# Kernel tuning notes

Measured on AMD Instinct MI355X. Metric: run time of the kernel, lower is better.

The kernel has to match this reference:

```python
import jax, jax.numpy as jnp
import numpy as np
import math

D_MODEL = 1024
N_HEAD = 16          # sub-heads per branch
N_BR = 4             # hardcoded n_branches
DH = D_MODEL // N_HEAD
H_TOT = N_BR * N_HEAD
B, T = 1, 1024
SCALE = math.pi / math.sqrt(3.0)
ATTNSCALE = DH ** -0.5


def _rope(x):
    # x: [B, H, T, D]; matches torch RoPE: even/odd split, concat halves
    t_len, d = x.shape[2], x.shape[-1]
    inv_freq = 1.0 / (10000.0 ** (jnp.arange(0, d, 2, dtype=jnp.float32) / d))
    freqs = jnp.arange(t_len, dtype=jnp.float32)[:, None] * inv_freq[None, :]  # [T, D/2]
    cos, sin = jnp.cos(freqs), jnp.sin(freqs)
    x1, x2 = x[..., 0::2], x[..., 1::2]
    return jnp.concatenate([-x2 * sin + x1 * cos, x1 * sin + x2 * cos], axis=-1)


def setup_inputs() -> dict:
    key = jax.random.key(0)
    ks = jax.random.split(key, 12)
    s = D_MODEL ** -0.5
    return {
        "X": jax.random.normal(ks[0], (B, T, D_MODEL), jnp.float32),
        "W_Q": jax.random.normal(ks[1], (D_MODEL, D_MODEL * N_BR), jnp.float32) * s,
        "b_Q": jax.random.normal(ks[2], (D_MODEL * N_BR,), jnp.float32) * 0.02,
        "W_K": jax.random.normal(ks[3], (D_MODEL, D_MODEL), jnp.float32) * s,
        "b_K": jax.random.normal(ks[4], (D_MODEL,), jnp.float32) * 0.02,
        "W_V": jax.random.normal(ks[5], (D_MODEL, D_MODEL), jnp.float32) * s,
        "b_V": jax.random.normal(ks[6], (D_MODEL,), jnp.float32) * 0.02,
        "sink_scalars": jax.random.uniform(ks[7], (H_TOT,), jnp.float32, 0.0, 0.1),
        "v_nulls": jax.random.normal(ks[8], (N_BR, D_MODEL), jnp.float32) * 0.02,
        "W_O": jax.random.normal(ks[9], (N_BR, D_MODEL, D_MODEL), jnp.float32) * s,
        "W_O_bias": jax.random.normal(ks[10], (N_BR, D_MODEL), jnp.float32) * 0.02,
    }


def reference(X, W_Q, b_Q, W_K, b_K, W_V, b_V, sink_scalars, v_nulls, W_O, W_O_bias):
    Bv, Tv, C = X.shape
    # projections -> [B, H, T, Dh]
    q = (X @ W_Q + b_Q).reshape(Bv, Tv, H_TOT, DH).transpose(0, 2, 1, 3)
    k_base = (X @ W_K + b_K).reshape(Bv, Tv, N_HEAD, DH).transpose(0, 2, 1, 3)
    v_base = (X @ W_V + b_V).reshape(Bv, Tv, N_HEAD, DH).transpose(0, 2, 1, 3)
    k = jnp.tile(k_base, (1, N_BR, 1, 1))
    v = jnp.tile(v_base, (1, N_BR, 1, 1))
    q, k = _rope(q), _rope(k)

    scores = jnp.einsum("bhtd,bhsd->bhts", q, k) * ATTNSCALE
    key_self = jnp.clip(jnp.sum(k * k, axis=-1), 1e-6, None)      # [B,H,S]
    w = jax.nn.softplus(scores / jnp.sqrt(key_self)[:, :, None, :])
    causal = jnp.tril(jnp.ones((Tv, Tv), bool))                    # [T,S]
    w = jnp.where(causal, w, 0.0)
    w = w * jax.nn.sigmoid(SCALE * w)
    sinks = sink_scalars.reshape(1, H_TOT, 1, 1)
    w = jnp.where(w < sinks, 0.0, w)
    # concat-with-sink renormalization, expressed without the concat
    total = jnp.sum(w, axis=-1, keepdims=True) + sinks + 1e-6      # [B,H,T,1]
    probs_tokens = w / total
    probs_sink = sinks / total                                     # [B,H,T,1]

    out = jnp.einsum("bhts,bhsd->bhtd", probs_tokens, v)
    v_null = v_nulls.reshape(H_TOT, DH)[None, :, None, :]          # [1,H,1,Dh]
    out = out + probs_sink * v_null

    context = out.reshape(Bv, N_BR, N_HEAD, Tv, DH).transpose(0, 1, 3, 2, 4)
    context = context.reshape(Bv, N_BR, Tv, C)
    y = jnp.einsum("bntc,ncd->bntd", context, W_O) + W_O_bias[None, :, None, :]
    return y.mean(axis=1)
```

## Files before the change

kernel.cpp:

```cpp
#include <hip/hip_runtime.h>
#include <math.h>

typedef __attribute__((ext_vector_type(4))) float  f32x4;
typedef __attribute__((ext_vector_type(8))) short  bf16x8;
typedef __attribute__((ext_vector_type(4))) short  s16x4;

#define SQUISH_SCALE 1.8137993642342178f

__device__ __forceinline__ float b2f(short u) {
    union { float f; unsigned b; } v; v.b = ((unsigned)(unsigned short)u) << 16; return v.f;
}
__device__ __forceinline__ short f2b(float f) {
    union { float f; unsigned b; } v; v.f = f;
    unsigned r = (v.b + 0x7FFFu + ((v.b >> 16) & 1u)) >> 16;
    return (short)r;
}
__device__ __forceinline__ unsigned cvt_pk_bf16(float lo, float hi) {
    unsigned r;
    asm("v_cvt_pk_bf16_f32 %0, %1, %2" : "=v"(r) : "v"(lo), "v"(hi));
    return r;
}
__device__ __forceinline__ void gll16(const void* g, void* l) {
    __builtin_amdgcn_global_load_lds((const __attribute__((address_space(1))) void*)g,
                                     (__attribute__((address_space(3))) void*)l, 16, 0, 0);
}
__device__ __forceinline__ void gll4(const void* g, void* l) {
    __builtin_amdgcn_global_load_lds((const __attribute__((address_space(1))) void*)g,
                                     (__attribute__((address_space(3))) void*)l, 4, 0, 0);
}

__device__ __forceinline__ void do_transpose(const float* __restrict__ src, int R, int C,
                                             short* __restrict__ dst, float scale,
                                             int c0, int r0, float (*tile)[65], int tid) {
    #pragma unroll
    for (int it = 0; it < 4; ++it) {
        int lin = it * 256 + tid;
        int r = lin >> 4, c4 = lin & 15;
        f32x4 v = *(const f32x4*)(src + (size_t)(r0 + r) * C + c0 + c4 * 4);
        #pragma unroll
        for (int k = 0; k < 4; ++k) tile[r][c4 * 4 + k] = v[k];
    }
    __syncthreads();
    #pragma unroll
    for (int it = 0; it < 4; ++it) {
        int lin = it * 256 + tid;
        int c = lin >> 4, rq = lin & 15;
        s16x4 o;
        #pragma unroll
        for (int k = 0; k < 4; ++k) o[k] = f2b(tile[rq * 4 + k][c] * scale);
        *(s16x4*)(dst + (size_t)(c0 + c) * R + r0 + rq * 4) = o;
    }
}

__global__ __launch_bounds__(256) void prep_kernel(
    const float* __restrict__ X, const float* __restrict__ W_Q, const float* __restrict__ W_K,
    const float* __restrict__ W_V, const float* __restrict__ W_O,
    const float* __restrict__ bQ, const float* __restrict__ bK, const float* __restrict__ bV,
    const float* __restrict__ bO,
    short* __restrict__ Xb, short* __restrict__ WbT, short* __restrict__ WoT,
    float* __restrict__ biasQKV, float* __restrict__ out) {
    __shared__ float tile[64][65];
    const int bid = blockIdx.x, tid = threadIdx.x;
    if (bid < 256) {
        int i = (bid * 256 + tid) * 16;
        #pragma unroll
        for (int k = 0; k < 4; ++k) {
            f32x4 v = *(const f32x4*)(X + i + k * 4);
            s16x4 o;
            o.x = f2b(v.x); o.y = f2b(v.y); o.z = f2b(v.z); o.w = f2b(v.w);
            *(s16x4*)(Xb + i + k * 4) = o;
        }
    } else if (bid < 1280) {
        int b2 = bid - 256;
        do_transpose(W_Q, 1024, 4096, WbT, 1.f, (b2 & 63) * 64, (b2 >> 6) * 64, tile, tid);
    } else if (bid < 1536) {
        int b2 = bid - 1280;
        do_transpose(W_K, 1024, 1024, WbT + 4096 * 1024, 1.f, (b2 & 15) * 64, (b2 >> 4) * 64, tile, tid);
    } else if (bid < 1792) {
        int b2 = bid - 1536;
        do_transpose(W_V, 1024, 1024, WbT + 5120 * 1024, 1.f, (b2 & 15) * 64, (b2 >> 4) * 64, tile, tid);
    } else if (bid < 2816) {
        int b2 = bid - 1792;
        do_transpose(W_O, 4096, 1024, WoT, 0.25f, (b2 & 15) * 64, (b2 >> 4) * 64, tile, tid);
    } else if (bid < 2840) {
        int i = (bid - 2816) * 256 + tid;
        if (i < 4096)      biasQKV[i] = bQ[i];
        else if (i < 5120) biasQKV[i] = bK[i - 4096];
        else               biasQKV[i] = bV[i - 5120];
    } else {
        int i = ((bid - 2840) * 256 + tid) * 4;
        f32x4 v;
        #pragma unroll
        for (int k = 0; k < 4; ++k) {
            int c = (i + k) & 1023;
            v[k] = 0.25f * (bO[c] + bO[1024 + c] + bO[2048 + c] + bO[3072 + c]);
        }
        *(f32x4*)(out + i) = v;
    }
}

__global__ __launch_bounds__(256) void gemm_bt_kernel(
    const short* __restrict__ A, const short* __restrict__ BT,
    const float* __restrict__ bias, short* __restrict__ outB,
    int M, int N, int K) {
    __shared__ short lA[2][128][64];
    __shared__ short lB[2][128][64];
    const int tid = threadIdx.x;
    const int lane = tid & 63, wave = tid >> 6;
    const int l15 = lane & 15, l4 = lane >> 4;
    const int wr = wave >> 1, wc = wave & 1;
    const int n0 = blockIdx.x * 128, m0 = blockIdx.y * 128;

    f32x4 acc[4][4];
    const f32x4 fz = {0.f, 0.f, 0.f, 0.f};
    #pragma unroll
    for (int m = 0; m < 4; ++m)
        #pragma unroll
        for (int n = 0; n < 4; ++n) acc[m][n] = fz;

#define GSTAGE(k0_, b_) do {                                                   \
    _Pragma("unroll")                                                          \
    for (int it = 0; it < 4; ++it) {                                           \
        int lin0 = it * 256 + wave * 64;                                       \
        int lin = lin0 + lane;                                                 \
        int r = lin >> 3, c = (lin & 7) ^ (r & 7);                             \
        gll16(A  + (size_t)(m0 + r) * K + (k0_) + c * 8, (char*)lA[b_] + lin0 * 16); \
        gll16(BT + (size_t)(n0 + r) * K + (k0_) + c * 8, (char*)lB[b_] + lin0 * 16); \
    } } while (0)

    GSTAGE(0, 0);
    int cur = 0;
    for (int k0 = 0; k0 < K; k0 += 64) {
        if (k0 + 64 < K) {
            GSTAGE(k0 + 64, cur ^ 1);
            asm volatile("s_waitcnt vmcnt(8) lgkmcnt(0)" ::: "memory");
        } else {
            asm volatile("s_waitcnt vmcnt(0) lgkmcnt(0)" ::: "memory");
        }
        __builtin_amdgcn_s_barrier();
        #pragma unroll
        for (int kk = 0; kk < 2; ++kk) {
            bf16x8 af[4], bf_[4];
            #pragma unroll
            for (int m = 0; m < 4; ++m) {
                int row = wr * 64 + m * 16 + l15;
                int ch = (kk * 4 + l4) ^ (row & 7);
                af[m] = *(const bf16x8*)&lA[cur][row][ch << 3];
            }
            #pragma unroll
            for (int n = 0; n < 4; ++n) {
                int row = wc * 64 + n * 16 + l15;
                int ch = (kk * 4 + l4) ^ (row & 7);
                bf_[n] = *(const bf16x8*)&lB[cur][row][ch << 3];
            }
            #pragma unroll
            for (int m = 0; m < 4; ++m)
                #pragma unroll
                for (int n = 0; n < 4; ++n)
                    acc[m][n] = __builtin_amdgcn_mfma_f32_16x16x32_bf16(af[m], bf_[n], acc[m][n], 0, 0, 0);
        }
        asm volatile("" ::: "memory");
        __builtin_amdgcn_s_barrier();
        cur ^= 1;
    }
#undef GSTAGE
    #pragma unroll
    for (int m = 0; m < 4; ++m)
        #pragma unroll
        for (int n = 0; n < 4; ++n)
            #pragma unroll
            for (int r = 0; r < 4; ++r) {
                int row = m0 + wr * 64 + m * 16 + l4 * 4 + r;
                int col = n0 + wc * 64 + n * 16 + l15;
                outB[(size_t)row * N + col] = f2b(acc[m][n][r] + bias[col]);
            }
}

__global__ __launch_bounds__(256) void gemm_bt_splitk_kernel(
    const short* __restrict__ A, const short* __restrict__ BT,
    float* __restrict__ out, int M, int N, int K, int KSLICE) {
    __shared__ short lA[2][128][64];
    __shared__ short lB[2][128][64];
    const int tid = threadIdx.x;
    const int lane = tid & 63, wave = tid >> 6;
    const int l15 = lane & 15, l4 = lane >> 4;
    const int wr = wave >> 1, wc = wave & 1;
    const int n0 = blockIdx.x * 128, m0 = blockIdx.y * 128;
    const int kbeg = blockIdx.z * KSLICE, kend = kbeg + KSLICE;

    f32x4 acc[4][4];
    const f32x4 fz = {0.f, 0.f, 0.f, 0.f};
    #pragma unroll
    for (int m = 0; m < 4; ++m)
        #pragma unroll
        for (int n = 0; n < 4; ++n) acc[m][n] = fz;

#define GSTAGE(k0_, b_) do {                                                   \
    _Pragma("unroll")                                                          \
    for (int it = 0; it < 4; ++it) {                                           \
        int lin0 = it * 256 + wave * 64;                                       \
        int lin = lin0 + lane;                                                 \
        int r = lin >> 3, c = (lin & 7) ^ (r & 7);                             \
        gll16(A  + (size_t)(m0 + r) * K + (k0_) + c * 8, (char*)lA[b_] + lin0 * 16); \
        gll16(BT + (size_t)(n0 + r) * K + (k0_) + c * 8, (char*)lB[b_] + lin0 * 16); \
    } } while (0)

    GSTAGE(kbeg, 0);
    int cur = 0;
    for (int k0 = kbeg; k0 < kend; k0 += 64) {
        if (k0 + 64 < kend) {
            GSTAGE(k0 + 64, cur ^ 1);
            asm volatile("s_waitcnt vmcnt(8) lgkmcnt(0)" ::: "memory");
        } else {
            asm volatile("s_waitcnt vmcnt(0) lgkmcnt(0)" ::: "memory");
        }
        __builtin_amdgcn_s_barrier();
        #pragma unroll
        for (int kk = 0; kk < 2; ++kk) {
            bf16x8 af[4], bf_[4];
            #pragma unroll
            for (int m = 0; m < 4; ++m) {
                int row = wr * 64 + m * 16 + l15;
                int ch = (kk * 4 + l4) ^ (row & 7);
                af[m] = *(const bf16x8*)&lA[cur][row][ch << 3];
            }
            #pragma unroll
            for (int n = 0; n < 4; ++n) {
                int row = wc * 64 + n * 16 + l15;
                int ch = (kk * 4 + l4) ^ (row & 7);
                bf_[n] = *(const bf16x8*)&lB[cur][row][ch << 3];
            }
            #pragma unroll
            for (int m = 0; m < 4; ++m)
                #pragma unroll
                for (int n = 0; n < 4; ++n)
                    acc[m][n] = __builtin_amdgcn_mfma_f32_16x16x32_bf16(af[m], bf_[n], acc[m][n], 0, 0, 0);
        }
        asm volatile("" ::: "memory");
        __builtin_amdgcn_s_barrier();
        cur ^= 1;
    }
#undef GSTAGE
    #pragma unroll
    for (int m = 0; m < 4; ++m)
        #pragma unroll
        for (int n = 0; n < 4; ++n)
            #pragma unroll
            for (int r = 0; r < 4; ++r) {
                int row = m0 + wr * 64 + m * 16 + l4 * 4 + r;
                int col = n0 + wc * 64 + n * 16 + l15;
                unsafeAtomicAdd(&out[(size_t)row * N + col], acc[m][n][r]);
            }
}

__global__ __launch_bounds__(256) void rope_vt_kernel(short* __restrict__ QKVb,
                                                      float* __restrict__ ksr,
                                                      short* __restrict__ Vtb) {
    __shared__ short tile[64][72];
    const int bid = blockIdx.x, tid = threadIdx.x;
    if (bid < 1280) {
        int base = bid * 256 + tid;
        #pragma unroll
        for (int it = 0; it < 8; ++it) {
            int item = base + it * 327680;
            int j = item & 31;
            int rem = item >> 5;
            int head = rem % 80;
            int t = rem / 80;
            short* p;
            if (head < 64) p = QKVb + (size_t)t * 6144 + head * 64;
            else           p = QKVb + (size_t)t * 6144 + 4096 + (head - 64) * 64;
            float x1 = b2f(p[2 * j]), x2 = b2f(p[2 * j + 1]);
            float freq = (float)t * __builtin_exp2f(-(float)j * 0.41524101186092033f);
            float sn = __sinf(freq), cs = __cosf(freq);
            float o1 = x1 * cs - x2 * sn;
            float o2 = x1 * sn + x2 * cs;
            p[j]      = f2b(o1);
            p[32 + j] = f2b(o2);
            if (head >= 64) {
                float ss = o1 * o1 + o2 * o2;
                #pragma unroll
                for (int off = 16; off; off >>= 1) ss += __shfl_xor(ss, off, 32);
                if (j == 0) ksr[(head - 64) * 1024 + t] = 0.125f * rsqrtf(fmaxf(ss, 1e-6f));
            }
        }
    } else {
        int b2 = bid - 1280;
        int h = b2 >> 4, t0 = (b2 & 15) * 64;
        #pragma unroll
        for (int it = 0; it < 16; ++it) {
            int lin = it * 256 + tid;
            int r = lin >> 6, d = lin & 63;
            tile[r][d] = QKVb[(size_t)(t0 + r) * 6144 + 5120 + h * 64 + d];
        }
        __syncthreads();
        #pragma unroll
        for (int it = 0; it < 16; ++it) {
            int lin = it * 256 + tid;
            int d = lin >> 6, c = lin & 63;
            Vtb[(size_t)(h * 64 + d) * 1024 + t0 + c] = tile[c][d];
        }
    }
}

__global__ __launch_bounds__(256, 3) void attn_kernel(
    const short* __restrict__ QKVb, const short* __restrict__ Vtb,
    const float* __restrict__ ksr, const float* __restrict__ sinks,
    const float* __restrict__ vnulls, short* __restrict__ Ob) {
    __shared__ short lK[2][64][64];
    __shared__ short lV[2][64][64];
    __shared__ float lks[2][64];
    __shared__ float lvn[64];
    __shared__ short lP[4][16][64];

    const int tid = threadIdx.x;
    const int lane = tid & 63, wave = tid >> 6;
    const int l15 = lane & 15, l4 = lane >> 4;
    const int h = blockIdx.x;
    const int qt = 15 - blockIdx.y;
    const int h16 = h & 15;
    const int t0 = qt * 64;
    const float sink = sinks[h];
    if (tid < 64) lvn[tid] = vnulls[h * 64 + tid];

    const int q_abs = t0 + wave * 16 + l15;
    bf16x8 aq[2];
    #pragma unroll
    for (int kk = 0; kk < 2; ++kk)
        aq[kk] = *(const bf16x8*)(QKVb + (size_t)q_abs * 6144 + h * 64 + kk * 32 + l4 * 8);

    const f32x4 fz = {0.f, 0.f, 0.f, 0.f};
    f32x4 acc_o[4];
    #pragma unroll
    for (int n = 0; n < 4; ++n) acc_o[n] = fz;
    float tot = 0.f;

#define ASTAGE(s0_, b_) do {                                                          \
    int lin0 = wave * 64;                                                             \
    int lin = lin0 + lane;                                                            \
    int r = lin >> 3, c = (lin & 7) ^ (r & 7);                                        \
    gll16(QKVb + (size_t)((s0_) + r) * 6144 + 4096 + h16 * 64 + c * 8, (char*)lK[b_] + lin0 * 16); \
    gll16(Vtb + (size_t)(h16 * 64 + r) * 1024 + (s0_) + c * 8,         (char*)lV[b_] + lin0 * 16); \
    lin0 += 256; lin = lin0 + lane; r = lin >> 3; c = (lin & 7) ^ (r & 7);            \
    gll16(QKVb + (size_t)((s0_) + r) * 6144 + 4096 + h16 * 64 + c * 8, (char*)lK[b_] + lin0 * 16); \
    gll16(Vtb + (size_t)(h16 * 64 + r) * 1024 + (s0_) + c * 8,         (char*)lV[b_] + lin0 * 16); \
    gll4(ksr + h16 * 1024 + (s0_) + lane, (char*)lks[b_]);                            \
} while (0)

    const int nkt = qt + 1;
    ASTAGE(0, 0);
    int cur = 0;
    for (int kt = 0; kt < nkt; ++kt) {
        int s0 = kt * 64;
        if (kt + 1 < nkt) {
            ASTAGE(s0 + 64, cur ^ 1);
            asm volatile("s_waitcnt vmcnt(5) lgkmcnt(0)" ::: "memory");
        } else {
            asm volatile("s_waitcnt vmcnt(0) lgkmcnt(0)" ::: "memory");
        }
        __builtin_amdgcn_s_barrier();

        f32x4 accs[4];
        #pragma unroll
        for (int n = 0; n < 4; ++n) accs[n] = fz;
        #pragma unroll
        for (int kk = 0; kk < 2; ++kk) {
            bf16x8 bk[4];
            #pragma unroll
            for (int n = 0; n < 4; ++n) {
                int row = n * 16 + l15;
                int ch = (kk * 4 + l4) ^ (row & 7);
                bk[n] = *(const bf16x8*)&lK[cur][row][ch << 3];
            }
            #pragma unroll
            for (int n = 0; n < 4; ++n)
                accs[n] = __builtin_amdgcn_mfma_f32_16x16x32_bf16(bk[n], aq[kk], accs[n], 0, 0, 0);
        }

        #pragma unroll
        for (int n = 0; n < 4; ++n) {
            f32x4 ksv = *(const f32x4*)&lks[cur][n * 16 + l4 * 4];
            float w4[4];
            #pragma unroll
            for (int r = 0; r < 4; ++r) {
                int k_abs = s0 + n * 16 + l4 * 4 + r;
                float z = accs[n][r] * ksv[r];
                float e = __expf(-fabsf(z));
                float w = fmaxf(z, 0.f) + __logf(1.f + e);
                w = (k_abs <= q_abs) ? w : 0.f;
                float g = __expf(-SQUISH_SCALE * w);
                w = w * __builtin_amdgcn_rcpf(1.f + g);
                w = (w >= sink) ? w : 0.f;
                tot += w;
                w4[r] = w;
            }
            unsigned pa = cvt_pk_bf16(w4[0], w4[1]);
            unsigned pb = cvt_pk_bf16(w4[2], w4[3]);
            int ch = (2 * n + (l4 >> 1)) ^ (l15 & 7);
            uint2 val; val.x = pa; val.y = pb;
            *(uint2*)&lP[wave][l15][ch * 8 + (l4 & 1) * 4] = val;
        }

        #pragma unroll
        for (int kk = 0; kk < 2; ++kk) {
            bf16x8 ap = *(const bf16x8*)&lP[wave][l15][((kk * 4 + l4) ^ (l15 & 7)) << 3];
            bf16x8 bv[4];
            #pragma unroll
            for (int n = 0; n < 4; ++n) {
                int row = n * 16 + l15;
                int ch = (kk * 4 + l4) ^ (row & 7);
                bv[n] = *(const bf16x8*)&lV[cur][row][ch << 3];
            }
            #pragma unroll
            for (int n = 0; n < 4; ++n)
                acc_o[n] = __builtin_amdgcn_mfma_f32_16x16x32_bf16(ap, bv[n], acc_o[n], 0, 0, 0);
        }
        asm volatile("" ::: "memory");
        __builtin_amdgcn_s_barrier();
        cur ^= 1;
    }
#undef ASTAGE

    tot += __shfl_xor(tot, 16, 64);
    tot += __shfl_xor(tot, 32, 64);
    float tq[4];
    #pragma unroll
    for (int r = 0; r < 4; ++r) tq[r] = __shfl(tot, l4 * 4 + r, 64);

    #pragma unroll
    for (int r = 0; r < 4; ++r) {
        float inv = __builtin_amdgcn_rcpf(tq[r] + sink + 1e-6f);
        int trow = t0 + wave * 16 + l4 * 4 + r;
        #pragma unroll
        for (int n = 0; n < 4; ++n) {
            int d = n * 16 + l15;
            float val = (acc_o[n][r] + sink * lvn[d]) * inv;
            Ob[(size_t)trow * 4096 + h * 64 + d] = f2b(val);
        }
    }
}

extern "C" void kernel_launch(void* const* d_in, const int* in_sizes, int n_in,
                              void* d_out, int out_size, void* d_ws, size_t ws_size,
                              hipStream_t stream) {
    const float* X        = (const float*)d_in[0];
    const float* W_Q      = (const float*)d_in[1];
    const float* b_Q      = (const float*)d_in[2];
    const float* W_K      = (const float*)d_in[3];
    const float* b_K      = (const float*)d_in[4];
    const float* W_V      = (const float*)d_in[5];
    const float* b_V      = (const float*)d_in[6];
    const float* sinks    = (const float*)d_in[7];
    const float* v_nulls  = (const float*)d_in[8];
    const float* W_O      = (const float*)d_in[9];
    const float* W_O_bias = (const float*)d_in[10];
    float* out = (float*)d_out;
    char* ws = (char*)d_ws;

    short* Xb        = (short*)(ws + 0);
    short* WbT       = (short*)(ws + 2097152);
    short* WoT       = (short*)(ws + 14680064);
    short* QKVb      = (short*)(ws + 23068672);
    short* Vtb       = (short*)(ws + 35651584);
    short* Ob        = (short*)(ws + 37748736);
    float* ksr       = (float*)(ws + 46137344);
    float* biasQKV   = (float*)(ws + 46202880);

    prep_kernel<<<3864, 256, 0, stream>>>(X, W_Q, W_K, W_V, W_O, b_Q, b_K, b_V, W_O_bias,
                                          Xb, WbT, WoT, biasQKV, out);
    gemm_bt_kernel<<<dim3(48, 8), 256, 0, stream>>>(Xb, WbT, biasQKV, QKVb, 1024, 6144, 1024);
    rope_vt_kernel<<<1536, 256, 0, stream>>>(QKVb, ksr, Vtb);
    attn_kernel<<<dim3(64, 16), 256, 0, stream>>>(QKVb, Vtb, ksr, sinks, v_nulls, Ob);
    gemm_bt_splitk_kernel<<<dim3(8, 8, 8), 256, 0, stream>>>(Ob, WoT, out, 1024, 1024, 4096, 512);
}
```

Measured before the change: 207.9 us.

## Split long causal attention tiles across blocks, shrink GEMM tiles, use exp2 softplus

The attention grid now uses 24 slots per head. Query tiles 8 to 15 have their key range split across two blocks, which combine partial outputs and row sums with float atomics into a zeroed buffer, and a new norm kernel then normalizes them. The aim is to balance the causal work per block and fill more CUs. Both GEMMs move to 64x128 tiles with twice the blocks and a launch-bound occupancy hint. The attention inner loop drops its K/V double buffering in favour of single-buffered loads with full waits, and softplus and the sigmoid are rewritten in base 2 with the log2e factor folded into ksr. In exchange it adds a memset, atomic traffic, an extra kernel, and loses the load/compute overlap inside attention.

```diff
diff --git a/kernel.cpp b/kernel.cpp
--- a/kernel.cpp
+++ b/kernel.cpp
@@ -5,7 +5,8 @@
 typedef __attribute__((ext_vector_type(8))) short  bf16x8;
 typedef __attribute__((ext_vector_type(4))) short  s16x4;
 
-#define SQUISH_SCALE 1.8137993642342178f
+#define SQUISH_U 1.8137993642342178f
+#define LN2F     0.69314718055994531f
 
 __device__ __forceinline__ float b2f(short u) {
     union { float f; unsigned b; } v; v.b = ((unsigned)(unsigned short)u) << 16; return v.f;
@@ -99,155 +100,120 @@
     }
 }
 
-__global__ __launch_bounds__(256) void gemm_bt_kernel(
+#define GSTAGE_64x128(k0_, b_) do {                                            \
+    _Pragma("unroll")                                                          \
+    for (int it = 0; it < 2; ++it) {                                           \
+        int lin0 = it * 256 + wave * 64;                                       \
+        int lin = lin0 + lane;                                                 \
+        int r = lin >> 3, c = (lin & 7) ^ (r & 7);                             \
+        gll16(A + (size_t)(m0 + r) * K + (k0_) + c * 8, (char*)lA[b_] + lin0 * 16); \
+    }                                                                          \
+    _Pragma("unroll")                                                          \
+    for (int it = 0; it < 4; ++it) {                                           \
+        int lin0 = it * 256 + wave * 64;                                       \
+        int lin = lin0 + lane;                                                 \
+        int r = lin >> 3, c = (lin & 7) ^ (r & 7);                             \
+        gll16(BT + (size_t)(n0 + r) * K + (k0_) + c * 8, (char*)lB[b_] + lin0 * 16); \
+    } } while (0)
+
+#define GEMM_CORE_64x128(kbeg_, kend_)                                         \
+    GSTAGE_64x128(kbeg_, 0);                                                   \
+    int cur = 0;                                                               \
+    for (int k0 = (kbeg_); k0 < (kend_); k0 += 64) {                           \
+        if (k0 + 64 < (kend_)) {                                               \
+            GSTAGE_64x128(k0 + 64, cur ^ 1);                                   \
+            asm volatile("s_waitcnt vmcnt(6) lgkmcnt(0)" ::: "memory");        \
+        } else {                                                               \
+            asm volatile("s_waitcnt vmcnt(0) lgkmcnt(0)" ::: "memory");        \
+        }                                                                      \
+        __builtin_amdgcn_s_barrier();                                          \
+        _Pragma("unroll")                                                      \
+        for (int kk = 0; kk < 2; ++kk) {                                       \
+            bf16x8 af[2], bf_[4];                                              \
+            _Pragma("unroll")                                                  \
+            for (int m = 0; m < 2; ++m) {                                      \
+                int row = wr * 32 + m * 16 + l15;                              \
+                int ch = (kk * 4 + l4) ^ (row & 7);                            \
+                af[m] = *(const bf16x8*)&lA[cur][row][ch << 3];                \
+            }                                                                  \
+            _Pragma("unroll")                                                  \
+            for (int n = 0; n < 4; ++n) {                                      \
+                int row = wc * 64 + n * 16 + l15;                              \
+                int ch = (kk * 4 + l4) ^ (row & 7);                            \
+                bf_[n] = *(const bf16x8*)&lB[cur][row][ch << 3];               \
+            }                                                                  \
+            _Pragma("unroll")                                                  \
+            for (int m = 0; m < 2; ++m)                                        \
+                _Pragma("unroll")                                              \
+                for (int n = 0; n < 4; ++n)                                    \
+                    acc[m][n] = __builtin_amdgcn_mfma_f32_16x16x32_bf16(af[m], bf_[n], acc[m][n], 0, 0, 0); \
+        }                                                                      \
+        asm volatile("" ::: "memory");                                         \
+        __builtin_amdgcn_s_barrier();                                          \
+        cur ^= 1;                                                              \
+    }
+
+__global__ __launch_bounds__(256, 3) void gemm_qkv_kernel(
     const short* __restrict__ A, const short* __restrict__ BT,
     const float* __restrict__ bias, short* __restrict__ outB,
     int M, int N, int K) {
-    __shared__ short lA[2][128][64];
+    __shared__ short lA[2][64][64];
     __shared__ short lB[2][128][64];
     const int tid = threadIdx.x;
     const int lane = tid & 63, wave = tid >> 6;
     const int l15 = lane & 15, l4 = lane >> 4;
     const int wr = wave >> 1, wc = wave & 1;
-    const int n0 = blockIdx.x * 128, m0 = blockIdx.y * 128;
-
-    f32x4 acc[4][4];
+    const int n0 = blockIdx.x * 128, m0 = blockIdx.y * 64;
+
+    f32x4 acc[2][4];
     const f32x4 fz = {0.f, 0.f, 0.f, 0.f};
     #pragma unroll
-    for (int m = 0; m < 4; ++m)
+    for (int m = 0; m < 2; ++m)
         #pragma unroll
         for (int n = 0; n < 4; ++n) acc[m][n] = fz;
 
-#define GSTAGE(k0_, b_) do {                                                   \
-    _Pragma("unroll")                                                          \
-    for (int it = 0; it < 4; ++it) {                                           \
-        int lin0 = it * 256 + wave * 64;                                       \
-        int lin = lin0 + lane;                                                 \
-        int r = lin >> 3, c = (lin & 7) ^ (r & 7);                             \
-        gll16(A  + (size_t)(m0 + r) * K + (k0_) + c * 8, (char*)lA[b_] + lin0 * 16); \
-        gll16(BT + (size_t)(n0 + r) * K + (k0_) + c * 8, (char*)lB[b_] + lin0 * 16); \
-    } } while (0)
-
-    GSTAGE(0, 0);
-    int cur = 0;
-    for (int k0 = 0; k0 < K; k0 += 64) {
-        if (k0 + 64 < K) {
-            GSTAGE(k0 + 64, cur ^ 1);
-            asm volatile("s_waitcnt vmcnt(8) lgkmcnt(0)" ::: "memory");
-        } else {
-            asm volatile("s_waitcnt vmcnt(0) lgkmcnt(0)" ::: "memory");
-        }
-        __builtin_amdgcn_s_barrier();
-        #pragma unroll
-        for (int kk = 0; kk < 2; ++kk) {
-            bf16x8 af[4], bf_[4];
-            #pragma unroll
-            for (int m = 0; m < 4; ++m) {
-                int row = wr * 64 + m * 16 + l15;
-                int ch = (kk * 4 + l4) ^ (row & 7);
-                af[m] = *(const bf16x8*)&lA[cur][row][ch << 3];
-            }
-            #pragma unroll
-            for (int n = 0; n < 4; ++n) {
-                int row = wc * 64 + n * 16 + l15;
-                int ch = (kk * 4 + l4) ^ (row & 7);
-                bf_[n] = *(const bf16x8*)&lB[cur][row][ch << 3];
-            }
-            #pragma unroll
-            for (int m = 0; m < 4; ++m)
-                #pragma unroll
-                for (int n = 0; n < 4; ++n)
-                    acc[m][n] = __builtin_amdgcn_mfma_f32_16x16x32_bf16(af[m], bf_[n], acc[m][n], 0, 0, 0);
-        }
-        asm volatile("" ::: "memory");
-        __builtin_amdgcn_s_barrier();
-        cur ^= 1;
-    }
-#undef GSTAGE
-    #pragma unroll
-    for (int m = 0; m < 4; ++m)
+    GEMM_CORE_64x128(0, K);
+
+    #pragma unroll
+    for (int m = 0; m < 2; ++m)
         #pragma unroll
         for (int n = 0; n < 4; ++n)
             #pragma unroll
             for (int r = 0; r < 4; ++r) {
-                int row = m0 + wr * 64 + m * 16 + l4 * 4 + r;
+                int row = m0 + wr * 32 + m * 16 + l4 * 4 + r;
                 int col = n0 + wc * 64 + n * 16 + l15;
                 outB[(size_t)row * N + col] = f2b(acc[m][n][r] + bias[col]);
             }
 }
 
-__global__ __launch_bounds__(256) void gemm_bt_splitk_kernel(
+__global__ __launch_bounds__(256, 3) void gemm_op_kernel(
     const short* __restrict__ A, const short* __restrict__ BT,
     float* __restrict__ out, int M, int N, int K, int KSLICE) {
-    __shared__ short lA[2][128][64];
+    __shared__ short lA[2][64][64];
     __shared__ short lB[2][128][64];
     const int tid = threadIdx.x;
     const int lane = tid & 63, wave = tid >> 6;
     const int l15 = lane & 15, l4 = lane >> 4;
     const int wr = wave >> 1, wc = wave & 1;
-    const int n0 = blockIdx.x * 128, m0 = blockIdx.y * 128;
+    const int n0 = blockIdx.x * 128, m0 = blockIdx.y * 64;
     const int kbeg = blockIdx.z * KSLICE, kend = kbeg + KSLICE;
 
-    f32x4 acc[4][4];
+    f32x4 acc[2][4];
     const f32x4 fz = {0.f, 0.f, 0.f, 0.f};
     #pragma unroll
-    for (int m = 0; m < 4; ++m)
+    for (int m = 0; m < 2; ++m)
         #pragma unroll
         for (int n = 0; n < 4; ++n) acc[m][n] = fz;
 
-#define GSTAGE(k0_, b_) do {                                                   \
-    _Pragma("unroll")                                                          \
-    for (int it = 0; it < 4; ++it) {                                           \
-        int lin0 = it * 256 + wave * 64;                                       \
-        int lin = lin0 + lane;                                                 \
-        int r = lin >> 3, c = (lin & 7) ^ (r & 7);                             \
-        gll16(A  + (size_t)(m0 + r) * K + (k0_) + c * 8, (char*)lA[b_] + lin0 * 16); \
-        gll16(BT + (size_t)(n0 + r) * K + (k0_) + c * 8, (char*)lB[b_] + lin0 * 16); \
-    } } while (0)
-
-    GSTAGE(kbeg, 0);
-    int cur = 0;
-    for (int k0 = kbeg; k0 < kend; k0 += 64) {
-        if (k0 + 64 < kend) {
-            GSTAGE(k0 + 64, cur ^ 1);
-            asm volatile("s_waitcnt vmcnt(8) lgkmcnt(0)" ::: "memory");
-        } else {
-            asm volatile("s_waitcnt vmcnt(0) lgkmcnt(0)" ::: "memory");
-        }
-        __builtin_amdgcn_s_barrier();
-        #pragma unroll
-        for (int kk = 0; kk < 2; ++kk) {
-            bf16x8 af[4], bf_[4];
-            #pragma unroll
-            for (int m = 0; m < 4; ++m) {
-                int row = wr * 64 + m * 16 + l15;
-                int ch = (kk * 4 + l4) ^ (row & 7);
-                af[m] = *(const bf16x8*)&lA[cur][row][ch << 3];
-            }
-            #pragma unroll
-            for (int n = 0; n < 4; ++n) {
-                int row = wc * 64 + n * 16 + l15;
-                int ch = (kk * 4 + l4) ^ (row & 7);
-                bf_[n] = *(const bf16x8*)&lB[cur][row][ch << 3];
-            }
-            #pragma unroll
-            for (int m = 0; m < 4; ++m)
-                #pragma unroll
-                for (int n = 0; n < 4; ++n)
-                    acc[m][n] = __builtin_amdgcn_mfma_f32_16x16x32_bf16(af[m], bf_[n], acc[m][n], 0, 0, 0);
-        }
-        asm volatile("" ::: "memory");
-        __builtin_amdgcn_s_barrier();
-        cur ^= 1;
-    }
-#undef GSTAGE
-    #pragma unroll
-    for (int m = 0; m < 4; ++m)
+    GEMM_CORE_64x128(kbeg, kend);
+
+    #pragma unroll
+    for (int m = 0; m < 2; ++m)
         #pragma unroll
         for (int n = 0; n < 4; ++n)
             #pragma unroll
             for (int r = 0; r < 4; ++r) {
-                int row = m0 + wr * 64 + m * 16 + l4 * 4 + r;
+                int row = m0 + wr * 32 + m * 16 + l4 * 4 + r;
                 int col = n0 + wc * 64 + n * 16 + l15;
                 unsafeAtomicAdd(&out[(size_t)row * N + col], acc[m][n][r]);
             }
@@ -281,7 +247,7 @@
                 float ss = o1 * o1 + o2 * o2;
                 #pragma unroll
                 for (int off = 16; off; off >>= 1) ss += __shfl_xor(ss, off, 32);
-                if (j == 0) ksr[(head - 64) * 1024 + t] = 0.125f * rsqrtf(fmaxf(ss, 1e-6f));
+                if (j == 0) ksr[(head - 64) * 1024 + t] = 0.18033688011112042f * rsqrtf(fmaxf(ss, 1e-6f));
             }
         }
     } else {
@@ -303,13 +269,18 @@
     }
 }
 
-__global__ __launch_bounds__(256, 3) void attn_kernel(
+__constant__ __device__ const signed char TQT[24] = {15,15,14, 7,14,13,13,12, 6,12,11,11,10, 5,10, 9, 9, 8, 4, 8, 3, 2, 1, 0};
+__constant__ __device__ const signed char TKB[24] = { 0, 8, 0, 0, 8, 0, 7, 0, 0, 7, 0, 6, 0, 0, 6, 0, 5, 0, 0, 5, 0, 0, 0, 0};
+__constant__ __device__ const signed char TKE[24] = { 8,16, 8, 8,15, 7,14, 7, 7,13, 6,12, 6, 6,11, 5,10, 5, 5, 9, 4, 3, 2, 1};
+
+__global__ __launch_bounds__(256, 6) void attn_kernel(
     const short* __restrict__ QKVb, const short* __restrict__ Vtb,
     const float* __restrict__ ksr, const float* __restrict__ sinks,
-    const float* __restrict__ vnulls, short* __restrict__ Ob) {
-    __shared__ short lK[2][64][64];
-    __shared__ short lV[2][64][64];
-    __shared__ float lks[2][64];
+    const float* __restrict__ vnulls, short* __restrict__ Ob,
+    float* __restrict__ Of, float* __restrict__ totf) {
+    __shared__ short lK[64][64];
+    __shared__ short lV[64][64];
+    __shared__ float lks[64];
     __shared__ float lvn[64];
     __shared__ short lP[4][16][64];
 
@@ -317,7 +288,9 @@
     const int lane = tid & 63, wave = tid >> 6;
     const int l15 = lane & 15, l4 = lane >> 4;
     const int h = blockIdx.x;
-    const int qt = 15 - blockIdx.y;
+    const int slot = blockIdx.y;
+    const int qt = TQT[slot], kb = TKB[slot], ke = TKE[slot];
+    const bool single = (kb == 0) && (ke == qt + 1);
     const int h16 = h & 15;
     const int t0 = qt * 64;
     const float sink = sinks[h];
@@ -335,30 +308,24 @@
     for (int n = 0; n < 4; ++n) acc_o[n] = fz;
     float tot = 0.f;
 
-#define ASTAGE(s0_, b_) do {                                                          \
+#define ASTAGE(s0_) do {                                                              \
     int lin0 = wave * 64;                                                             \
     int lin = lin0 + lane;                                                            \
     int r = lin >> 3, c = (lin & 7) ^ (r & 7);                                        \
-    gll16(QKVb + (size_t)((s0_) + r) * 6144 + 4096 + h16 * 64 + c * 8, (char*)lK[b_] + lin0 * 16); \
-    gll16(Vtb + (size_t)(h16 * 64 + r) * 1024 + (s0_) + c * 8,         (char*)lV[b_] + lin0 * 16); \
+    gll16(QKVb + (size_t)((s0_) + r) * 6144 + 4096 + h16 * 64 + c * 8, (char*)lK + lin0 * 16); \
+    gll16(Vtb + (size_t)(h16 * 64 + r) * 1024 + (s0_) + c * 8,         (char*)lV + lin0 * 16); \
     lin0 += 256; lin = lin0 + lane; r = lin >> 3; c = (lin & 7) ^ (r & 7);            \
-    gll16(QKVb + (size_t)((s0_) + r) * 6144 + 4096 + h16 * 64 + c * 8, (char*)lK[b_] + lin0 * 16); \
-    gll16(Vtb + (size_t)(h16 * 64 + r) * 1024 + (s0_) + c * 8,         (char*)lV[b_] + lin0 * 16); \
-    gll4(ksr + h16 * 1024 + (s0_) + lane, (char*)lks[b_]);                            \
+    gll16(QKVb + (size_t)((s0_) + r) * 6144 + 4096 + h16 * 64 + c * 8, (char*)lK + lin0 * 16); \
+    gll16(Vtb + (size_t)(h16 * 64 + r) * 1024 + (s0_) + c * 8,         (char*)lV + lin0 * 16); \
+    gll4(ksr + h16 * 1024 + (s0_) + lane, (char*)lks);                                \
 } while (0)
 
-    const int nkt = qt + 1;
-    ASTAGE(0, 0);
-    int cur = 0;
-    for (int kt = 0; kt < nkt; ++kt) {
+    for (int kt = kb; kt < ke; ++kt) {
         int s0 = kt * 64;
-        if (kt + 1 < nkt) {
-            ASTAGE(s0 + 64, cur ^ 1);
-            asm volatile("s_waitcnt vmcnt(5) lgkmcnt(0)" ::: "memory");
-        } else {
-            asm volatile("s_waitcnt vmcnt(0) lgkmcnt(0)" ::: "memory");
-        }
-        __builtin_amdgcn_s_barrier();
+        __syncthreads();
+        ASTAGE(s0);
+        asm volatile("s_waitcnt vmcnt(0)" ::: "memory");
+        __syncthreads();
 
         f32x4 accs[4];
         #pragma unroll
@@ -370,7 +337,7 @@
             for (int n = 0; n < 4; ++n) {
                 int row = n * 16 + l15;
                 int ch = (kk * 4 + l4) ^ (row & 7);
-                bk[n] = *(const bf16x8*)&lK[cur][row][ch << 3];
+                bk[n] = *(const bf16x8*)&lK[row][ch << 3];
             }
             #pragma unroll
             for (int n = 0; n < 4; ++n)
@@ -379,17 +346,17 @@
 
         #pragma unroll
         for (int n = 0; n < 4; ++n) {
-            f32x4 ksv = *(const f32x4*)&lks[cur][n * 16 + l4 * 4];
+            f32x4 ksv = *(const f32x4*)&lks[n * 16 + l4 * 4];
             float w4[4];
             #pragma unroll
             for (int r = 0; r < 4; ++r) {
                 int k_abs = s0 + n * 16 + l4 * 4 + r;
-                float z = accs[n][r] * ksv[r];
-                float e = __expf(-fabsf(z));
-                float w = fmaxf(z, 0.f) + __logf(1.f + e);
-                w = (k_abs <= q_abs) ? w : 0.f;
-                float g = __expf(-SQUISH_SCALE * w);
-                w = w * __builtin_amdgcn_rcpf(1.f + g);
+                float zz = accs[n][r] * ksv[r];
+                float t = __builtin_amdgcn_exp2f(zz);
+                float u = __builtin_amdgcn_logf(1.f + t);
+                u = (k_abs <= q_abs) ? u : 0.f;
+                float g = __builtin_amdgcn_rcpf(1.f + __builtin_amdgcn_exp2f(-SQUISH_U * u));
+                float w = LN2F * u * g;
                 w = (w >= sink) ? w : 0.f;
                 tot += w;
                 w4[r] = w;
@@ -409,35 +376,64 @@
             for (int n = 0; n < 4; ++n) {
                 int row = n * 16 + l15;
                 int ch = (kk * 4 + l4) ^ (row & 7);
-                bv[n] = *(const bf16x8*)&lV[cur][row][ch << 3];
+                bv[n] = *(const bf16x8*)&lV[row][ch << 3];
             }
             #pragma unroll
             for (int n = 0; n < 4; ++n)
                 acc_o[n] = __builtin_amdgcn_mfma_f32_16x16x32_bf16(ap, bv[n], acc_o[n], 0, 0, 0);
         }
-        asm volatile("" ::: "memory");
-        __builtin_amdgcn_s_barrier();
-        cur ^= 1;
     }
 #undef ASTAGE
 
     tot += __shfl_xor(tot, 16, 64);
     tot += __shfl_xor(tot, 32, 64);
-    float tq[4];
-    #pragma unroll
-    for (int r = 0; r < 4; ++r) tq[r] = __shfl(tot, l4 * 4 + r, 64);
-
-    #pragma unroll
-    for (int r = 0; r < 4; ++r) {
-        float inv = __builtin_amdgcn_rcpf(tq[r] + sink + 1e-6f);
-        int trow = t0 + wave * 16 + l4 * 4 + r;
-        #pragma unroll
-        for (int n = 0; n < 4; ++n) {
-            int d = n * 16 + l15;
-            float val = (acc_o[n][r] + sink * lvn[d]) * inv;
-            Ob[(size_t)trow * 4096 + h * 64 + d] = f2b(val);
-        }
-    }
+
+    if (single) {
+        float tq[4];
+        #pragma unroll
+        for (int r = 0; r < 4; ++r) tq[r] = __shfl(tot, l4 * 4 + r, 64);
+        #pragma unroll
+        for (int r = 0; r < 4; ++r) {
+            float inv = __builtin_amdgcn_rcpf(tq[r] + sink + 1e-6f);
+            int trow = t0 + wave * 16 + l4 * 4 + r;
+            #pragma unroll
+            for (int n = 0; n < 4; ++n) {
+                int d = n * 16 + l15;
+                float val = (acc_o[n][r] + sink * lvn[d]) * inv;
+                Ob[(size_t)trow * 4096 + h * 64 + d] = f2b(val);
+            }
+        }
+    } else {
+        if (lane < 16)
+            unsafeAtomicAdd(&totf[h * 512 + (t0 - 512) + wave * 16 + l15], tot);
+        #pragma unroll
+        for (int r = 0; r < 4; ++r) {
+            int pr = h * 512 + (t0 - 512) + wave * 16 + l4 * 4 + r;
+            #pragma unroll
+            for (int n = 0; n < 4; ++n)
+                unsafeAtomicAdd(&Of[(size_t)pr * 64 + n * 16 + l15], acc_o[n][r]);
+        }
+    }
+}
+
+__global__ __launch_bounds__(256) void norm_kernel(
+    const float* __restrict__ Of, const float* __restrict__ totf,
+    const float* __restrict__ sinks, const float* __restrict__ vnulls,
+    short* __restrict__ Ob) {
+    int gid = blockIdx.x * 256 + threadIdx.x;
+    int i4 = gid * 4;
+    int row = i4 >> 6;
+    int d0 = i4 & 63;
+    int h = row >> 9;
+    int t = 512 + (row & 511);
+    float sink = sinks[h];
+    float inv = __builtin_amdgcn_rcpf(totf[row] + sink + 1e-6f);
+    f32x4 o = *(const f32x4*)(Of + i4);
+    s16x4 rs;
+    #pragma unroll
+    for (int k = 0; k < 4; ++k)
+        rs[k] = f2b((o[k] + sink * vnulls[h * 64 + d0 + k]) * inv);
+    *(s16x4*)(Ob + (size_t)t * 4096 + h * 64 + d0) = rs;
 }
 
 extern "C" void kernel_launch(void* const* d_in, const int* in_sizes, int n_in,
@@ -465,11 +461,15 @@
     short* Ob        = (short*)(ws + 37748736);
     float* ksr       = (float*)(ws + 46137344);
     float* biasQKV   = (float*)(ws + 46202880);
+    float* Of        = (float*)(ws + 2097152);
+    float* totf      = Of + 64 * 512 * 64;
 
     prep_kernel<<<3864, 256, 0, stream>>>(X, W_Q, W_K, W_V, W_O, b_Q, b_K, b_V, W_O_bias,
                                           Xb, WbT, WoT, biasQKV, out);
-    gemm_bt_kernel<<<dim3(48, 8), 256, 0, stream>>>(Xb, WbT, biasQKV, QKVb, 1024, 6144, 1024);
+    gemm_qkv_kernel<<<dim3(48, 16), 256, 0, stream>>>(Xb, WbT, biasQKV, QKVb, 1024, 6144, 1024);
     rope_vt_kernel<<<1536, 256, 0, stream>>>(QKVb, ksr, Vtb);
-    attn_kernel<<<dim3(64, 16), 256, 0, stream>>>(QKVb, Vtb, ksr, sinks, v_nulls, Ob);
-    gemm_bt_splitk_kernel<<<dim3(8, 8, 8), 256, 0, stream>>>(Ob, WoT, out, 1024, 1024, 4096, 512);
-}
+    hipMemsetAsync(Of, 0, (size_t)(64 * 512 * 64 + 64 * 512) * sizeof(float), stream);
+    attn_kernel<<<dim3(64, 24), 256, 0, stream>>>(QKVb, Vtb, ksr, sinks, v_nulls, Ob, Of, totf);
+    norm_kernel<<<2048, 256, 0, stream>>>(Of, totf, sinks, v_nulls, Ob);
+    gemm_op_kernel<<<dim3(8, 16, 8), 256, 0, stream>>>(Ob, WoT, out, 1024, 1024, 4096, 512);
+}
```

Result: no change. 204.7 us (-1.5%).
